# Kernel tuning notes

Hardware: AMD Instinct MI355X
Metric: run time of the kernel (lower is better)

## Reference

```python
import jax, jax.numpy as jnp
import numpy as np
import math

D_EMBED = 1536
N_HEADS = 12
D_AUG = D_EMBED // 3          # 512
HEAD_DIM = D_EMBED // N_HEADS # 128
ROPE_BASE = 10000.0


def apply_rope(x):
    # x: [B, S, H, D], interleaved-pair RoPE (torchtune convention)
    B, S, H, D = x.shape
    half = D // 2
    freqs = 1.0 / (ROPE_BASE ** (jnp.arange(0, D, 2, dtype=jnp.float32) / D))  # [half]
    ang = jnp.arange(S, dtype=jnp.float32)[:, None] * freqs[None, :]           # [S, half]
    cos = jnp.cos(ang)[None, :, None, :]  # [1,S,1,half]
    sin = jnp.sin(ang)[None, :, None, :]
    xr = x.reshape(B, S, H, half, 2)
    x1, x2 = xr[..., 0], xr[..., 1]
    out = jnp.stack([x1 * cos - x2 * sin, x1 * sin + x2 * cos], axis=-1)
    return out.reshape(B, S, H, D).astype(x.dtype)


def setup_inputs() -> dict:
    key = jax.random.key(0)
    ks = jax.random.split(key, 7)
    B, S = 2, 2048
    s = 0.02
    return {
        "q": jax.random.normal(ks[0], (B, S, D_EMBED), jnp.float32),
        "k": jax.random.normal(ks[1], (B, S, D_EMBED), jnp.float32),
        "v": jax.random.normal(ks[2], (B, S, D_EMBED), jnp.float32),
        "W_q": jax.random.normal(ks[3], (D_EMBED, D_EMBED), jnp.float32) * s,
        "W_k": jax.random.normal(ks[4], (D_EMBED, D_EMBED), jnp.float32) * s,
        "W_v": jax.random.normal(ks[5], (D_AUG, D_AUG), jnp.float32) * s,
        "W_o": jax.random.normal(ks[6], (D_EMBED, D_EMBED), jnp.float32) * s,
    }


def reference(q, k, v, W_q, W_k, W_v, W_o):
    # Dropout layers are identity in eval mode.
    B, S, _ = q.shape
    qh = q @ W_q.T                                     # [B,S,D]
    kh = k @ W_k.T
    v_mid = v[:, :, D_AUG:2 * D_AUG] @ W_v.T           # [B,S,D_AUG]
    vh = jnp.concatenate(
        [v_mid, jnp.zeros_like(v_mid), jnp.zeros_like(v_mid)], axis=-1)  # [B,S,D]

    qh = qh.reshape(B, S, N_HEADS, HEAD_DIM)
    kh = kh.reshape(B, S, N_HEADS, HEAD_DIM)
    vh = vh.reshape(B, S, N_HEADS, HEAD_DIM)

    qh = apply_rope(qh)
    kh = apply_rope(kh)

    scores = jnp.einsum('bqhd,bkhd->bhqk', qh, kh) / math.sqrt(HEAD_DIM)
    causal = jnp.triu(jnp.ones((S, S), dtype=bool), k=1)
    scores = jnp.where(causal[None, None], -jnp.inf, scores)
    probs = jax.nn.softmax(scores, axis=-1)

    attn = jnp.einsum('bhqk,bkhd->bqhd', probs, vh).reshape(B, S, D_EMBED)
    return attn @ W_o.T
```

## Files before the change

kernel.cpp:

```cpp
#include <hip/hip_runtime.h>
#include <hip/hip_bf16.h>

typedef __attribute__((ext_vector_type(8))) short short8;
typedef __attribute__((ext_vector_type(4))) short short4v;
typedef __attribute__((ext_vector_type(4))) float f32x4;

__device__ __forceinline__ short f2bf(float f) {
    union { float f; unsigned u; } v; v.f = f;
    unsigned r = (v.u + 0x7fffu + ((v.u >> 16) & 1u)) >> 16;
    return (short)r;
}
__device__ __forceinline__ float bf2f(short s) {
    union { unsigned u; float f; } v; v.u = ((unsigned)(unsigned short)s) << 16;
    return v.f;
}
__device__ __forceinline__ f32x4 zero4() { f32x4 z = {0.f, 0.f, 0.f, 0.f}; return z; }

__device__ __forceinline__ void gl16(const void* g, void* l) {
    __builtin_amdgcn_global_load_lds(
        (const __attribute__((address_space(1))) void*)g,
        (__attribute__((address_space(3))) void*)l, 16, 0, 0);
}

__global__ __launch_bounds__(256) void convertA_kernel(
    const float* __restrict__ q, const float* __restrict__ k,
    const float* __restrict__ Wq, const float* __restrict__ Wk,
    short* __restrict__ qb, short* __restrict__ kb,
    short* __restrict__ Wqb, short* __restrict__ Wkb)
{
    const int e0 = (blockIdx.x * 256 + threadIdx.x) * 8;
    const float* src; short* dst; int n;
    switch (blockIdx.z) {
    case 0:  n = 6291456; src = q + e0;  dst = qb;  break;
    case 1:  n = 6291456; src = k + e0;  dst = kb;  break;
    case 2:  n = 786432;  src = Wq + e0; dst = Wqb; break;
    default: n = 786432;  src = Wk + e0; dst = Wkb; break;
    }
    if (e0 >= n) return;
    float4 f0 = ((const float4*)src)[0];
    float4 f1 = ((const float4*)src)[1];
    short8 o;
    o[0]=f2bf(f0.x); o[1]=f2bf(f0.y); o[2]=f2bf(f0.z); o[3]=f2bf(f0.w);
    o[4]=f2bf(f1.x); o[5]=f2bf(f1.y); o[6]=f2bf(f1.z); o[7]=f2bf(f1.w);
    *(short8*)(dst + e0) = o;
}

template<bool ROPE>
__device__ __forceinline__ void gemm97_bf16out(
    const short* __restrict__ A, const short* __restrict__ B, short* __restrict__ Cp,
    int K, int lda, int ldb, int ldc, short* As, short* Bs)
{
    const int bm = blockIdx.y * 128;
    const int bn = blockIdx.x * 128;
    const int tid = threadIdx.x;
    const int w = tid >> 6;
    const int lane = tid & 63;
    const int l15 = lane & 15;
    const int quad = lane >> 4;
    const int wm = (w >> 1) * 64;
    const int wn = (w & 1) * 64;

    const int srow = w * 32 + (lane >> 2);
    const int scol = (lane & 3) * 8;
    const short* ga = A + (size_t)(bm + srow) * lda + scol;
    const short* gb = B + (size_t)(bn + srow) * ldb + scol;

    f32x4 acc[4][4];
#pragma unroll
    for (int i = 0; i < 4; i++)
#pragma unroll
        for (int j = 0; j < 4; j++) acc[i][j] = zero4();

    for (int k0 = 0; k0 < K; k0 += 64) {
        __syncthreads();
#pragma unroll
        for (int p = 0; p < 2; p++) {
            gl16(ga + k0 + p * 32,                    &As[p * 4096 + (w * 32) * 32]);
            gl16(ga + k0 + p * 32 + (size_t)16 * lda, &As[p * 4096 + (w * 32 + 16) * 32]);
            gl16(gb + k0 + p * 32,                    &Bs[p * 4096 + (w * 32) * 32]);
            gl16(gb + k0 + p * 32 + (size_t)16 * ldb, &Bs[p * 4096 + (w * 32 + 16) * 32]);
        }
        __syncthreads();

        short8 af[2][4], bf[2][4];
#pragma unroll
        for (int p = 0; p < 2; p++) {
#pragma unroll
            for (int i = 0; i < 4; i++)
                af[p][i] = *(const short8*)&As[p * 4096 + (wm + i * 16 + l15) * 32 + quad * 8];
#pragma unroll
            for (int j = 0; j < 4; j++)
                bf[p][j] = *(const short8*)&Bs[p * 4096 + (wn + j * 16 + l15) * 32 + quad * 8];
        }
#pragma unroll
        for (int i = 0; i < 4; i++)
#pragma unroll
            for (int j = 0; j < 4; j++) {
                acc[i][j] = __builtin_amdgcn_mfma_f32_16x16x32_bf16(af[0][i], bf[0][j], acc[i][j], 0, 0, 0);
                acc[i][j] = __builtin_amdgcn_mfma_f32_16x16x32_bf16(af[1][i], bf[1][j], acc[i][j], 0, 0, 0);
            }
    }

#pragma unroll
    for (int i = 0; i < 4; i++)
#pragma unroll
        for (int j = 0; j < 4; j++) {
            const int col = bn + wn + j * 16 + l15;
            const int row0 = bm + wm + i * 16 + quad * 4;
            if constexpr (ROPE) {
                const int pairi = (col & 127) >> 1;
                const float freq = exp2f(-(float)(2 * pairi) * (13.287712379549449f / 128.0f));
                const bool even = (l15 & 1) == 0;
#pragma unroll
                for (int r = 0; r < 4; r++) {
                    const float own = acc[i][j][r];
                    const float other = __shfl_xor(own, 1, 64);
                    const float pos = (float)((row0 + r) & 2047);
                    const float ang = pos * freq;
                    const float n = rintf(ang * 0.15915494309189535f);
                    const float rr = (ang - n * 6.28125f) - n * 1.9353071795864769e-3f;
                    float s, c;
                    __sincosf(rr, &s, &c);
                    const float x1 = even ? own : other;
                    const float x2 = even ? other : own;
                    const float res = even ? (x1 * c - x2 * s) : (x1 * s + x2 * c);
                    Cp[(size_t)(row0 + r) * ldc + col] = f2bf(res);
                }
            } else {
#pragma unroll
                for (int r = 0; r < 4; r++)
                    Cp[(size_t)(row0 + r) * ldc + col] = f2bf(acc[i][j][r]);
            }
        }
}

__device__ __forceinline__ void gemm_f32_bt_T(
    const float* __restrict__ A, const float* __restrict__ Bw, short* __restrict__ Cp,
    int K, int lda, int ldb, int ldc, short* As, short* Bs)
{
    const int bm = blockIdx.y * 128;
    const int bn = blockIdx.x * 128;
    const int tid = threadIdx.x;
    const int w = tid >> 6;
    const int lane = tid & 63;
    const int l15 = lane & 15;
    const int quad = lane >> 4;
    const int wm = (w >> 1) * 64;
    const int wn = (w & 1) * 64;
    const int srow = tid >> 1;
    const int scol = (tid & 1) * 16;

    f32x4 acc[4][4];
#pragma unroll
    for (int i = 0; i < 4; i++)
#pragma unroll
        for (int j = 0; j < 4; j++) acc[i][j] = zero4();

    for (int k0 = 0; k0 < K; k0 += 32) {
        __syncthreads();
        {
            const float* src = A + (size_t)(bm + srow) * lda + k0 + scol;
            short* dst = &As[srow * 40 + scol];
            const float4* s4 = (const float4*)src;
            float4 f0 = s4[0], f1 = s4[1], f2 = s4[2], f3 = s4[3];
            short8 t0, t1;
            t0[0]=f2bf(f0.x); t0[1]=f2bf(f0.y); t0[2]=f2bf(f0.z); t0[3]=f2bf(f0.w);
            t0[4]=f2bf(f1.x); t0[5]=f2bf(f1.y); t0[6]=f2bf(f1.z); t0[7]=f2bf(f1.w);
            t1[0]=f2bf(f2.x); t1[1]=f2bf(f2.y); t1[2]=f2bf(f2.z); t1[3]=f2bf(f2.w);
            t1[4]=f2bf(f3.x); t1[5]=f2bf(f3.y); t1[6]=f2bf(f3.z); t1[7]=f2bf(f3.w);
            *(short8*)dst = t0; *(short8*)(dst + 8) = t1;
        }
        {
            const float* src = Bw + (size_t)(bn + srow) * ldb + k0 + scol;
            short* dst = &Bs[srow * 40 + scol];
            const float4* s4 = (const float4*)src;
            float4 f0 = s4[0], f1 = s4[1], f2 = s4[2], f3 = s4[3];
            short8 t0, t1;
            t0[0]=f2bf(f0.x); t0[1]=f2bf(f0.y); t0[2]=f2bf(f0.z); t0[3]=f2bf(f0.w);
            t0[4]=f2bf(f1.x); t0[5]=f2bf(f1.y); t0[6]=f2bf(f1.z); t0[7]=f2bf(f1.w);
            t1[0]=f2bf(f2.x); t1[1]=f2bf(f2.y); t1[2]=f2bf(f2.z); t1[3]=f2bf(f2.w);
            t1[4]=f2bf(f3.x); t1[5]=f2bf(f3.y); t1[6]=f2bf(f3.z); t1[7]=f2bf(f3.w);
            *(short8*)dst = t0; *(short8*)(dst + 8) = t1;
        }
        __syncthreads();

        short8 af[4], bfr[4];
#pragma unroll
        for (int i = 0; i < 4; i++)
            af[i] = *(const short8*)&As[(wm + i * 16 + l15) * 40 + quad * 8];
#pragma unroll
        for (int j = 0; j < 4; j++)
            bfr[j] = *(const short8*)&Bs[(wn + j * 16 + l15) * 40 + quad * 8];
#pragma unroll
        for (int i = 0; i < 4; i++)
#pragma unroll
            for (int j = 0; j < 4; j++)
                acc[i][j] = __builtin_amdgcn_mfma_f32_16x16x32_bf16(af[i], bfr[j], acc[i][j], 0, 0, 0);
    }

#pragma unroll
    for (int i = 0; i < 4; i++)
#pragma unroll
        for (int j = 0; j < 4; j++) {
            const int col = bn + wn + j * 16 + l15;
            const int row0 = bm + wm + i * 16 + quad * 4;
            short4v p;
#pragma unroll
            for (int r = 0; r < 4; r++) p[r] = f2bf(acc[i][j][r]);
            *(short4v*)&Cp[(size_t)col * ldc + row0] = p;
        }
}

__device__ __forceinline__ void gemm_mixed_f32out(
    const short* __restrict__ A, const float* __restrict__ Bw, float* __restrict__ Cp,
    int K, int lda, int ldb, int ldc, short* As, short* Bs)
{
    const int bm = blockIdx.y * 128;
    const int bn = blockIdx.x * 128;
    const int tid = threadIdx.x;
    const int w = tid >> 6;
    const int lane = tid & 63;
    const int l15 = lane & 15;
    const int quad = lane >> 4;
    const int wm = (w >> 1) * 64;
    const int wn = (w & 1) * 64;
    const int srow = tid >> 1;
    const int scol = (tid & 1) * 16;

    f32x4 acc[4][4];
#pragma unroll
    for (int i = 0; i < 4; i++)
#pragma unroll
        for (int j = 0; j < 4; j++) acc[i][j] = zero4();

    for (int k0 = 0; k0 < K; k0 += 32) {
        __syncthreads();
        {
            const short* src = A + (size_t)(bm + srow) * lda + k0 + scol;
            short* dst = &As[srow * 40 + scol];
            const uint4* s4 = (const uint4*)src;
            uint4 a = s4[0], b = s4[1];
            *(uint4*)dst = a; *(uint4*)(dst + 8) = b;
        }
        {
            const float* src = Bw + (size_t)(bn + srow) * ldb + k0 + scol;
            short* dst = &Bs[srow * 40 + scol];
            const float4* s4 = (const float4*)src;
            float4 f0 = s4[0], f1 = s4[1], f2 = s4[2], f3 = s4[3];
            short8 t0, t1;
            t0[0]=f2bf(f0.x); t0[1]=f2bf(f0.y); t0[2]=f2bf(f0.z); t0[3]=f2bf(f0.w);
            t0[4]=f2bf(f1.x); t0[5]=f2bf(f1.y); t0[6]=f2bf(f1.z); t0[7]=f2bf(f1.w);
            t1[0]=f2bf(f2.x); t1[1]=f2bf(f2.y); t1[2]=f2bf(f2.z); t1[3]=f2bf(f2.w);
            t1[4]=f2bf(f3.x); t1[5]=f2bf(f3.y); t1[6]=f2bf(f3.z); t1[7]=f2bf(f3.w);
            *(short8*)dst = t0; *(short8*)(dst + 8) = t1;
        }
        __syncthreads();

        short8 af[4], bfr[4];
#pragma unroll
        for (int i = 0; i < 4; i++)
            af[i] = *(const short8*)&As[(wm + i * 16 + l15) * 40 + quad * 8];
#pragma unroll
        for (int j = 0; j < 4; j++)
            bfr[j] = *(const short8*)&Bs[(wn + j * 16 + l15) * 40 + quad * 8];
#pragma unroll
        for (int i = 0; i < 4; i++)
#pragma unroll
            for (int j = 0; j < 4; j++)
                acc[i][j] = __builtin_amdgcn_mfma_f32_16x16x32_bf16(af[i], bfr[j], acc[i][j], 0, 0, 0);
    }

#pragma unroll
    for (int i = 0; i < 4; i++)
#pragma unroll
        for (int j = 0; j < 4; j++) {
            const int col = bn + wn + j * 16 + l15;
            const int row0 = bm + wm + i * 16 + quad * 4;
#pragma unroll
            for (int r = 0; r < 4; r++)
                Cp[(size_t)(row0 + r) * ldc + col] = acc[i][j][r];
        }
}

__global__ __launch_bounds__(256) void proj_kernel(
    const short* __restrict__ qb, const short* __restrict__ kb, const float* __restrict__ v,
    const short* __restrict__ Wqb, const short* __restrict__ Wkb, const float* __restrict__ Wv,
    short* __restrict__ qh, short* __restrict__ kh, short* __restrict__ vT)
{
    __shared__ short smem[2][8192];
    switch (blockIdx.z) {
    case 0:  gemm97_bf16out<true>(qb, Wqb, qh, 1536, 1536, 1536, 512, smem[0], smem[1]); break;
    case 1:  gemm97_bf16out<true>(kb, Wkb, kh, 1536, 1536, 1536, 512, smem[0], smem[1]); break;
    default: gemm_f32_bt_T(v + 512, Wv, vT, 512, 1536, 512, 4096, smem[0], smem[1]); break;
    }
}

__global__ __launch_bounds__(256) void outproj_kernel(
    const short* __restrict__ attn, const float* __restrict__ Wo, float* __restrict__ out)
{
    __shared__ short smem[2][5120];
    gemm_mixed_f32out(attn, Wo, out, 512, 512, 1536, 1536, smem[0], smem[1]);
}

__global__ __launch_bounds__(256, 4) void flash_kernel(
    const short* __restrict__ qh, const short* __restrict__ kh,
    const short* __restrict__ vT, short* __restrict__ attn)
{
    __shared__ float Os[4][16][128];
    __shared__ short Ps[4][16 * 40];
    __shared__ float Lp[4][16];

    const int id = blockIdx.x;
    const int hb = id & 7;
    const int b = hb & 1;
    const int h = hb >> 1;
    const int s = id >> 3;
    const int m = s & 31;
    const int g = s >> 5;
    const int base = (g >> 1) * 32 + m;
    const int qt = (g & 1) ? (127 - base) : base;
    const int tid = threadIdx.x;
    const int w = tid >> 6;
    const int lane = tid & 63;
    const int l15 = lane & 15;
    const int quad = lane >> 4;

    const float scale = 0.08838834764831845f;
    const float MFIX = 24.0f;
    const short* kbp = kh + (size_t)(b * 2048) * 512 + h * 128;
    const short* vbp = vT + (size_t)(h * 128) * 4096 + b * 2048;
    short* pw = &Ps[w][0];

    const int q0 = qt * 16;
    const int ntiles = (q0 + 47) >> 5;

    const short* qrow = qh + (size_t)(b * 2048 + q0 + l15) * 512 + h * 128;
    short8 aq[4];
#pragma unroll
    for (int kk = 0; kk < 4; kk++)
        aq[kk] = *(const short8*)&qrow[kk * 32 + quad * 8];

    f32x4 o[8];
#pragma unroll
    for (int dt = 0; dt < 8; dt++) o[dt] = zero4();
    float lsum[4] = {0.f, 0.f, 0.f, 0.f};

    for (int t = w; t < ntiles; t += 4) {
        const int kb0 = t * 32;

        f32x4 sc[2];
#pragma unroll
        for (int ct = 0; ct < 2; ct++) {
            sc[ct] = zero4();
            const short* kr = kbp + (size_t)(kb0 + ct * 16 + l15) * 512;
#pragma unroll
            for (int kk = 0; kk < 4; kk++) {
                short8 bk = *(const short8*)&kr[kk * 32 + quad * 8];
                sc[ct] = __builtin_amdgcn_mfma_f32_16x16x32_bf16(aq[kk], bk, sc[ct], 0, 0, 0);
            }
        }

        short8 bv[8];
#pragma unroll
        for (int dt = 0; dt < 8; dt++)
            bv[dt] = *(const short8*)&vbp[(size_t)(dt * 16 + l15) * 4096 + kb0 + quad * 8];

        const int rbase = q0 + quad * 4;
        float p[2][4];
#pragma unroll
        for (int ct = 0; ct < 2; ct++) {
            const int kcol = kb0 + ct * 16 + l15;
#pragma unroll
            for (int r = 0; r < 4; r++) {
                const float e = __expf(sc[ct][r] * scale - MFIX);
                const float pv = (kcol > rbase + r) ? 0.0f : e;
                p[ct][r] = pv;
                lsum[r] += pv;
            }
        }

#pragma unroll
        for (int ct = 0; ct < 2; ct++)
#pragma unroll
            for (int r = 0; r < 4; r++)
                pw[(quad * 4 + r) * 40 + ct * 16 + l15] = f2bf(p[ct][r]);
        short8 ap = *(const short8*)&pw[l15 * 40 + quad * 8];

#pragma unroll
        for (int dt = 0; dt < 8; dt++)
            o[dt] = __builtin_amdgcn_mfma_f32_16x16x32_bf16(ap, bv[dt], o[dt], 0, 0, 0);
    }

#pragma unroll
    for (int r = 0; r < 4; r++) {
        float vsum = lsum[r];
#pragma unroll
        for (int off = 1; off < 16; off <<= 1)
            vsum += __shfl_xor(vsum, off, 64);
        if (l15 == 0) Lp[w][quad * 4 + r] = vsum;
#pragma unroll
        for (int dt = 0; dt < 8; dt++)
            Os[w][quad * 4 + r][dt * 16 + l15] = o[dt][r];
    }
    __syncthreads();

    {
        const int row = tid >> 4;
        const int d0 = (tid & 15) * 8;
        const float L = Lp[0][row] + Lp[1][row] + Lp[2][row] + Lp[3][row];
        const float rL = 1.0f / L;
        short8 ov;
#pragma unroll
        for (int j = 0; j < 8; j++) {
            const float osum = Os[0][row][d0 + j] + Os[1][row][d0 + j]
                             + Os[2][row][d0 + j] + Os[3][row][d0 + j];
            ov[j] = f2bf(osum * rL);
        }
        *(short8*)&attn[(size_t)(b * 2048 + q0 + row) * 512 + h * 128 + d0] = ov;
    }
}

extern "C" void kernel_launch(void* const* d_in, const int* in_sizes, int n_in,
                              void* d_out, int out_size, void* d_ws, size_t ws_size,
                              hipStream_t stream) {
    const float* q  = (const float*)d_in[0];
    const float* k  = (const float*)d_in[1];
    const float* v  = (const float*)d_in[2];
    const float* Wq = (const float*)d_in[3];
    const float* Wk = (const float*)d_in[4];
    const float* Wv = (const float*)d_in[5];
    const float* Wo = (const float*)d_in[6];
    float* out = (float*)d_out;

    const size_t MB = 1024 * 1024;
    char* ws = (char*)d_ws;
    short* qh   = (short*)(ws);
    short* kh   = (short*)(ws + 4 * MB);
    short* vT   = (short*)(ws + 8 * MB);
    short* Wqb  = (short*)(ws + 12 * MB);
    short* Wkb  = (short*)(ws + 13 * MB + 512 * 1024);
    short* attn = (short*)(ws + 12 * MB);
    short* qb   = (short*)d_out;
    short* kb   = (short*)((char*)d_out + 12 * MB);

    convertA_kernel<<<dim3(3072, 1, 4), 256, 0, stream>>>(q, k, Wq, Wk, qb, kb, Wqb, Wkb);
    proj_kernel<<<dim3(4, 32, 3), 256, 0, stream>>>(qb, kb, v, Wqb, Wkb, Wv, qh, kh, vT);
    flash_kernel<<<dim3(1024, 1, 1), 256, 0, stream>>>(qh, kh, vT, attn);
    outproj_kernel<<<dim3(12, 32, 1), 256, 0, stream>>>(attn, Wo, out);
}
```

Measured before the change: 256.7 us.

## Store K and V in MFMA-fragment layout and halve projection M-tile

The K and V projection epilogues now write outputs in a pre-swizzled fragment layout, 32-key tiles of 4096 shorts. The flash kernel can then load each MFMA operand as one contiguous 16-byte-per-lane read, instead of strided row gathers across 512- or 4096-element strides. The projection GEMMs also drop from 128-row to 64-row tiles, doubling the grid to improve occupancy and load balance. The trade-off is scattered short stores in the K epilogue and less reuse per block in the projection GEMMs.

```diff
diff --git a/kernel.cpp b/kernel.cpp
--- a/kernel.cpp
+++ b/kernel.cpp
@@ -45,29 +45,30 @@
     *(short8*)(dst + e0) = o;
 }
 
-template<bool ROPE>
-__device__ __forceinline__ void gemm97_bf16out(
+template<int MODE>
+__device__ __forceinline__ void gemm97_bm64(
     const short* __restrict__ A, const short* __restrict__ B, short* __restrict__ Cp,
     int K, int lda, int ldb, int ldc, short* As, short* Bs)
 {
-    const int bm = blockIdx.y * 128;
+    const int bm = blockIdx.y * 64;
     const int bn = blockIdx.x * 128;
     const int tid = threadIdx.x;
     const int w = tid >> 6;
     const int lane = tid & 63;
     const int l15 = lane & 15;
     const int quad = lane >> 4;
-    const int wm = (w >> 1) * 64;
+    const int wm = (w >> 1) * 32;
     const int wn = (w & 1) * 64;
 
-    const int srow = w * 32 + (lane >> 2);
-    const int scol = (lane & 3) * 8;
-    const short* ga = A + (size_t)(bm + srow) * lda + scol;
-    const short* gb = B + (size_t)(bn + srow) * ldb + scol;
-
-    f32x4 acc[4][4];
-#pragma unroll
-    for (int i = 0; i < 4; i++)
+    const int srA = w * 16 + (lane >> 2);
+    const int srB = w * 32 + (lane >> 2);
+    const int sc  = (lane & 3) * 8;
+    const short* ga = A + (size_t)(bm + srA) * lda + sc;
+    const short* gb = B + (size_t)(bn + srB) * ldb + sc;
+
+    f32x4 acc[2][4];
+#pragma unroll
+    for (int i = 0; i < 2; i++)
 #pragma unroll
         for (int j = 0; j < 4; j++) acc[i][j] = zero4();
 
@@ -75,25 +76,24 @@
         __syncthreads();
 #pragma unroll
         for (int p = 0; p < 2; p++) {
-            gl16(ga + k0 + p * 32,                    &As[p * 4096 + (w * 32) * 32]);
-            gl16(ga + k0 + p * 32 + (size_t)16 * lda, &As[p * 4096 + (w * 32 + 16) * 32]);
+            gl16(ga + k0 + p * 32,                    &As[p * 2048 + (w * 16) * 32]);
             gl16(gb + k0 + p * 32,                    &Bs[p * 4096 + (w * 32) * 32]);
             gl16(gb + k0 + p * 32 + (size_t)16 * ldb, &Bs[p * 4096 + (w * 32 + 16) * 32]);
         }
         __syncthreads();
 
-        short8 af[2][4], bf[2][4];
+        short8 af[2][2], bf[2][4];
 #pragma unroll
         for (int p = 0; p < 2; p++) {
 #pragma unroll
-            for (int i = 0; i < 4; i++)
-                af[p][i] = *(const short8*)&As[p * 4096 + (wm + i * 16 + l15) * 32 + quad * 8];
+            for (int i = 0; i < 2; i++)
+                af[p][i] = *(const short8*)&As[p * 2048 + (wm + i * 16 + l15) * 32 + quad * 8];
 #pragma unroll
             for (int j = 0; j < 4; j++)
                 bf[p][j] = *(const short8*)&Bs[p * 4096 + (wn + j * 16 + l15) * 32 + quad * 8];
         }
 #pragma unroll
-        for (int i = 0; i < 4; i++)
+        for (int i = 0; i < 2; i++)
 #pragma unroll
             for (int j = 0; j < 4; j++) {
                 acc[i][j] = __builtin_amdgcn_mfma_f32_16x16x32_bf16(af[0][i], bf[0][j], acc[i][j], 0, 0, 0);
@@ -102,42 +102,140 @@
     }
 
 #pragma unroll
-    for (int i = 0; i < 4; i++)
+    for (int i = 0; i < 2; i++)
 #pragma unroll
         for (int j = 0; j < 4; j++) {
             const int col = bn + wn + j * 16 + l15;
             const int row0 = bm + wm + i * 16 + quad * 4;
-            if constexpr (ROPE) {
-                const int pairi = (col & 127) >> 1;
-                const float freq = exp2f(-(float)(2 * pairi) * (13.287712379549449f / 128.0f));
-                const bool even = (l15 & 1) == 0;
-#pragma unroll
-                for (int r = 0; r < 4; r++) {
-                    const float own = acc[i][j][r];
-                    const float other = __shfl_xor(own, 1, 64);
-                    const float pos = (float)((row0 + r) & 2047);
-                    const float ang = pos * freq;
-                    const float n = rintf(ang * 0.15915494309189535f);
-                    const float rr = (ang - n * 6.28125f) - n * 1.9353071795864769e-3f;
-                    float s, c;
-                    __sincosf(rr, &s, &c);
-                    const float x1 = even ? own : other;
-                    const float x2 = even ? other : own;
-                    const float res = even ? (x1 * c - x2 * s) : (x1 * s + x2 * c);
+            const int pairi = (col & 127) >> 1;
+            const float freq = exp2f(-(float)(2 * pairi) * (13.287712379549449f / 128.0f));
+            const bool even = (l15 & 1) == 0;
+#pragma unroll
+            for (int r = 0; r < 4; r++) {
+                const float own = acc[i][j][r];
+                const float other = __shfl_xor(own, 1, 64);
+                const float pos = (float)((row0 + r) & 2047);
+                const float ang = pos * freq;
+                const float n = rintf(ang * 0.15915494309189535f);
+                const float rr = (ang - n * 6.28125f) - n * 1.9353071795864769e-3f;
+                float s, c;
+                __sincosf(rr, &s, &c);
+                const float x1 = even ? own : other;
+                const float x2 = even ? other : own;
+                const float res = even ? (x1 * c - x2 * s) : (x1 * s + x2 * c);
+                if constexpr (MODE == 1) {
                     Cp[(size_t)(row0 + r) * ldc + col] = f2bf(res);
+                } else {
+                    const int seq = row0 + r;
+                    const int b_ = seq >> 11;
+                    const int s2 = seq & 2047;
+                    Cp[(size_t)(b_ * 4 + (col >> 7)) * 262144 + (s2 >> 5) * 4096
+                       + ((s2 >> 4) & 1) * 2048 + ((col >> 5) & 3) * 512
+                       + ((col >> 3) & 3) * 128 + (s2 & 15) * 8 + (col & 7)] = f2bf(res);
                 }
-            } else {
-#pragma unroll
-                for (int r = 0; r < 4; r++)
-                    Cp[(size_t)(row0 + r) * ldc + col] = f2bf(acc[i][j][r]);
             }
         }
 }
 
-__device__ __forceinline__ void gemm_f32_bt_T(
+__device__ __forceinline__ void gemm_f32T_vF(
     const float* __restrict__ A, const float* __restrict__ Bw, short* __restrict__ Cp,
-    int K, int lda, int ldb, int ldc, short* As, short* Bs)
-{
+    int K, int lda, int ldb, short* As, short* Bs)
+{
+    const int bm = blockIdx.y * 64;
+    const int bn = blockIdx.x * 128;
+    const int tid = threadIdx.x;
+    const int w = tid >> 6;
+    const int lane = tid & 63;
+    const int l15 = lane & 15;
+    const int quad = lane >> 4;
+    const int wm = (w >> 1) * 32;
+    const int wn = (w & 1) * 64;
+    const int srA = tid >> 2;
+    const int scA = (tid & 3) * 8;
+    const int srB = tid >> 1;
+    const int scB = (tid & 1) * 16;
+
+    f32x4 acc[2][4];
+#pragma unroll
+    for (int i = 0; i < 2; i++)
+#pragma unroll
+        for (int j = 0; j < 4; j++) acc[i][j] = zero4();
+
+    for (int k0 = 0; k0 < K; k0 += 32) {
+        __syncthreads();
+        {
+            const float* src = A + (size_t)(bm + srA) * lda + k0 + scA;
+            short* dst = &As[srA * 40 + scA];
+            const float4* s4 = (const float4*)src;
+            float4 f0 = s4[0], f1 = s4[1];
+            short8 t0;
+            t0[0]=f2bf(f0.x); t0[1]=f2bf(f0.y); t0[2]=f2bf(f0.z); t0[3]=f2bf(f0.w);
+            t0[4]=f2bf(f1.x); t0[5]=f2bf(f1.y); t0[6]=f2bf(f1.z); t0[7]=f2bf(f1.w);
+            *(short8*)dst = t0;
+        }
+        {
+            const float* src = Bw + (size_t)(bn + srB) * ldb + k0 + scB;
+            short* dst = &Bs[srB * 40 + scB];
+            const float4* s4 = (const float4*)src;
+            float4 f0 = s4[0], f1 = s4[1], f2 = s4[2], f3 = s4[3];
+            short8 t0, t1;
+            t0[0]=f2bf(f0.x); t0[1]=f2bf(f0.y); t0[2]=f2bf(f0.z); t0[3]=f2bf(f0.w);
+            t0[4]=f2bf(f1.x); t0[5]=f2bf(f1.y); t0[6]=f2bf(f1.z); t0[7]=f2bf(f1.w);
+            t1[0]=f2bf(f2.x); t1[1]=f2bf(f2.y); t1[2]=f2bf(f2.z); t1[3]=f2bf(f2.w);
+            t1[4]=f2bf(f3.x); t1[5]=f2bf(f3.y); t1[6]=f2bf(f3.z); t1[7]=f2bf(f3.w);
+            *(short8*)dst = t0; *(short8*)(dst + 8) = t1;
+        }
+        __syncthreads();
+
+        short8 af[2], bfr[4];
+#pragma unroll
+        for (int i = 0; i < 2; i++)
+            af[i] = *(const short8*)&As[(wm + i * 16 + l15) * 40 + quad * 8];
+#pragma unroll
+        for (int j = 0; j < 4; j++)
+            bfr[j] = *(const short8*)&Bs[(wn + j * 16 + l15) * 40 + quad * 8];
+#pragma unroll
+        for (int i = 0; i < 2; i++)
+#pragma unroll
+            for (int j = 0; j < 4; j++)
+                acc[i][j] = __builtin_amdgcn_mfma_f32_16x16x32_bf16(af[i], bfr[j], acc[i][j], 0, 0, 0);
+    }
+
+#pragma unroll
+    for (int i = 0; i < 2; i++)
+#pragma unroll
+        for (int j = 0; j < 4; j++) {
+            const int col = bn + wn + j * 16 + l15;
+            const int row0 = bm + wm + i * 16 + quad * 4;
+            const int b_ = row0 >> 11;
+            const int s2 = row0 & 2047;
+            short4v p;
+#pragma unroll
+            for (int r = 0; r < 4; r++) p[r] = f2bf(acc[i][j][r]);
+            const size_t addr = (size_t)(b_ * 4 + (col >> 7)) * 262144 + (s2 >> 5) * 4096
+                              + ((col >> 4) & 7) * 512 + ((s2 >> 3) & 3) * 128
+                              + (col & 15) * 8 + (s2 & 7);
+            *(short4v*)&Cp[addr] = p;
+        }
+}
+
+__global__ __launch_bounds__(256) void proj_kernel(
+    const short* __restrict__ qb, const short* __restrict__ kb, const float* __restrict__ v,
+    const short* __restrict__ Wqb, const short* __restrict__ Wkb, const float* __restrict__ Wv,
+    short* __restrict__ qh, short* __restrict__ khF, short* __restrict__ vF)
+{
+    __shared__ short smem[12288];
+    switch (blockIdx.z) {
+    case 0:  gemm97_bm64<1>(qb, Wqb, qh,  1536, 1536, 1536, 512, smem, smem + 4096); break;
+    case 1:  gemm97_bm64<2>(kb, Wkb, khF, 1536, 1536, 1536, 512, smem, smem + 4096); break;
+    default: gemm_f32T_vF(v + 512, Wv, vF, 512, 1536, 512, smem, smem + 2560); break;
+    }
+}
+
+__global__ __launch_bounds__(256) void outproj_kernel(
+    const short* __restrict__ attn, const float* __restrict__ Wo, float* __restrict__ out)
+{
+    __shared__ short smem[2][5120];
     const int bm = blockIdx.y * 128;
     const int bn = blockIdx.x * 128;
     const int tid = threadIdx.x;
@@ -149,6 +247,9 @@
     const int wn = (w & 1) * 64;
     const int srow = tid >> 1;
     const int scol = (tid & 1) * 16;
+    short* As = smem[0];
+    short* Bs = smem[1];
+    const int K = 512, lda = 512, ldb = 1536, ldc = 1536;
 
     f32x4 acc[4][4];
 #pragma unroll
@@ -159,19 +260,14 @@
     for (int k0 = 0; k0 < K; k0 += 32) {
         __syncthreads();
         {
-            const float* src = A + (size_t)(bm + srow) * lda + k0 + scol;
+            const short* src = attn + (size_t)(bm + srow) * lda + k0 + scol;
             short* dst = &As[srow * 40 + scol];
-            const float4* s4 = (const float4*)src;
-            float4 f0 = s4[0], f1 = s4[1], f2 = s4[2], f3 = s4[3];
-            short8 t0, t1;
-            t0[0]=f2bf(f0.x); t0[1]=f2bf(f0.y); t0[2]=f2bf(f0.z); t0[3]=f2bf(f0.w);
-            t0[4]=f2bf(f1.x); t0[5]=f2bf(f1.y); t0[6]=f2bf(f1.z); t0[7]=f2bf(f1.w);
-            t1[0]=f2bf(f2.x); t1[1]=f2bf(f2.y); t1[2]=f2bf(f2.z); t1[3]=f2bf(f2.w);
-            t1[4]=f2bf(f3.x); t1[5]=f2bf(f3.y); t1[6]=f2bf(f3.z); t1[7]=f2bf(f3.w);
-            *(short8*)dst = t0; *(short8*)(dst + 8) = t1;
+            const uint4* s4 = (const uint4*)src;
+            uint4 a = s4[0], b = s4[1];
+            *(uint4*)dst = a; *(uint4*)(dst + 8) = b;
         }
         {
-            const float* src = Bw + (size_t)(bn + srow) * ldb + k0 + scol;
+            const float* src = Wo + (size_t)(bn + srow) * ldb + k0 + scol;
             short* dst = &Bs[srow * 40 + scol];
             const float4* s4 = (const float4*)src;
             float4 f0 = s4[0], f1 = s4[1], f2 = s4[2], f3 = s4[3];
@@ -204,107 +300,15 @@
         for (int j = 0; j < 4; j++) {
             const int col = bn + wn + j * 16 + l15;
             const int row0 = bm + wm + i * 16 + quad * 4;
-            short4v p;
-#pragma unroll
-            for (int r = 0; r < 4; r++) p[r] = f2bf(acc[i][j][r]);
-            *(short4v*)&Cp[(size_t)col * ldc + row0] = p;
-        }
-}
-
-__device__ __forceinline__ void gemm_mixed_f32out(
-    const short* __restrict__ A, const float* __restrict__ Bw, float* __restrict__ Cp,
-    int K, int lda, int ldb, int ldc, short* As, short* Bs)
-{
-    const int bm = blockIdx.y * 128;
-    const int bn = blockIdx.x * 128;
-    const int tid = threadIdx.x;
-    const int w = tid >> 6;
-    const int lane = tid & 63;
-    const int l15 = lane & 15;
-    const int quad = lane >> 4;
-    const int wm = (w >> 1) * 64;
-    const int wn = (w & 1) * 64;
-    const int srow = tid >> 1;
-    const int scol = (tid & 1) * 16;
-
-    f32x4 acc[4][4];
-#pragma unroll
-    for (int i = 0; i < 4; i++)
-#pragma unroll
-        for (int j = 0; j < 4; j++) acc[i][j] = zero4();
-
-    for (int k0 = 0; k0 < K; k0 += 32) {
-        __syncthreads();
-        {
-            const short* src = A + (size_t)(bm + srow) * lda + k0 + scol;
-            short* dst = &As[srow * 40 + scol];
-            const uint4* s4 = (const uint4*)src;
-            uint4 a = s4[0], b = s4[1];
-            *(uint4*)dst = a; *(uint4*)(dst + 8) = b;
-        }
-        {
-            const float* src = Bw + (size_t)(bn + srow) * ldb + k0 + scol;
-            short* dst = &Bs[srow * 40 + scol];
-            const float4* s4 = (const float4*)src;
-            float4 f0 = s4[0], f1 = s4[1], f2 = s4[2], f3 = s4[3];
-            short8 t0, t1;
-            t0[0]=f2bf(f0.x); t0[1]=f2bf(f0.y); t0[2]=f2bf(f0.z); t0[3]=f2bf(f0.w);
-            t0[4]=f2bf(f1.x); t0[5]=f2bf(f1.y); t0[6]=f2bf(f1.z); t0[7]=f2bf(f1.w);
-            t1[0]=f2bf(f2.x); t1[1]=f2bf(f2.y); t1[2]=f2bf(f2.z); t1[3]=f2bf(f2.w);
-            t1[4]=f2bf(f3.x); t1[5]=f2bf(f3.y); t1[6]=f2bf(f3.z); t1[7]=f2bf(f3.w);
-            *(short8*)dst = t0; *(short8*)(dst + 8) = t1;
-        }
-        __syncthreads();
-
-        short8 af[4], bfr[4];
-#pragma unroll
-        for (int i = 0; i < 4; i++)
-            af[i] = *(const short8*)&As[(wm + i * 16 + l15) * 40 + quad * 8];
-#pragma unroll
-        for (int j = 0; j < 4; j++)
-            bfr[j] = *(const short8*)&Bs[(wn + j * 16 + l15) * 40 + quad * 8];
-#pragma unroll
-        for (int i = 0; i < 4; i++)
-#pragma unroll
-            for (int j = 0; j < 4; j++)
-                acc[i][j] = __builtin_amdgcn_mfma_f32_16x16x32_bf16(af[i], bfr[j], acc[i][j], 0, 0, 0);
-    }
-
-#pragma unroll
-    for (int i = 0; i < 4; i++)
-#pragma unroll
-        for (int j = 0; j < 4; j++) {
-            const int col = bn + wn + j * 16 + l15;
-            const int row0 = bm + wm + i * 16 + quad * 4;
 #pragma unroll
             for (int r = 0; r < 4; r++)
-                Cp[(size_t)(row0 + r) * ldc + col] = acc[i][j][r];
-        }
-}
-
-__global__ __launch_bounds__(256) void proj_kernel(
-    const short* __restrict__ qb, const short* __restrict__ kb, const float* __restrict__ v,
-    const short* __restrict__ Wqb, const short* __restrict__ Wkb, const float* __restrict__ Wv,
-    short* __restrict__ qh, short* __restrict__ kh, short* __restrict__ vT)
-{
-    __shared__ short smem[2][8192];
-    switch (blockIdx.z) {
-    case 0:  gemm97_bf16out<true>(qb, Wqb, qh, 1536, 1536, 1536, 512, smem[0], smem[1]); break;
-    case 1:  gemm97_bf16out<true>(kb, Wkb, kh, 1536, 1536, 1536, 512, smem[0], smem[1]); break;
-    default: gemm_f32_bt_T(v + 512, Wv, vT, 512, 1536, 512, 4096, smem[0], smem[1]); break;
-    }
-}
-
-__global__ __launch_bounds__(256) void outproj_kernel(
-    const short* __restrict__ attn, const float* __restrict__ Wo, float* __restrict__ out)
-{
-    __shared__ short smem[2][5120];
-    gemm_mixed_f32out(attn, Wo, out, 512, 512, 1536, 1536, smem[0], smem[1]);
+                out[(size_t)(row0 + r) * ldc + col] = acc[i][j][r];
+        }
 }
 
 __global__ __launch_bounds__(256, 4) void flash_kernel(
-    const short* __restrict__ qh, const short* __restrict__ kh,
-    const short* __restrict__ vT, short* __restrict__ attn)
+    const short* __restrict__ qh, const short* __restrict__ khF,
+    const short* __restrict__ vF, short* __restrict__ attn)
 {
     __shared__ float Os[4][16][128];
     __shared__ short Ps[4][16 * 40];
@@ -327,9 +331,6 @@
 
     const float scale = 0.08838834764831845f;
     const float MFIX = 24.0f;
-    const short* kbp = kh + (size_t)(b * 2048) * 512 + h * 128;
-    const short* vbp = vT + (size_t)(h * 128) * 4096 + b * 2048;
-    short* pw = &Ps[w][0];
 
     const int q0 = qt * 16;
     const int ntiles = (q0 + 47) >> 5;
@@ -340,22 +341,28 @@
     for (int kk = 0; kk < 4; kk++)
         aq[kk] = *(const short8*)&qrow[kk * 32 + quad * 8];
 
+    const short* kfb = khF + (size_t)(b * 4 + h) * 262144 + lane * 8;
+    const short* vfb = vF  + (size_t)(b * 4 + h) * 262144 + lane * 8;
+
     f32x4 o[8];
 #pragma unroll
     for (int dt = 0; dt < 8; dt++) o[dt] = zero4();
     float lsum[4] = {0.f, 0.f, 0.f, 0.f};
 
+    short* pw = &Ps[w][0];
+
     for (int t = w; t < ntiles; t += 4) {
         const int kb0 = t * 32;
+        const short* kt_ = kfb + t * 4096;
+        const short* vt_ = vfb + t * 4096;
 
         f32x4 sc[2];
 #pragma unroll
         for (int ct = 0; ct < 2; ct++) {
             sc[ct] = zero4();
-            const short* kr = kbp + (size_t)(kb0 + ct * 16 + l15) * 512;
 #pragma unroll
             for (int kk = 0; kk < 4; kk++) {
-                short8 bk = *(const short8*)&kr[kk * 32 + quad * 8];
+                short8 bk = *(const short8*)&kt_[ct * 2048 + kk * 512];
                 sc[ct] = __builtin_amdgcn_mfma_f32_16x16x32_bf16(aq[kk], bk, sc[ct], 0, 0, 0);
             }
         }
@@ -363,7 +370,7 @@
         short8 bv[8];
 #pragma unroll
         for (int dt = 0; dt < 8; dt++)
-            bv[dt] = *(const short8*)&vbp[(size_t)(dt * 16 + l15) * 4096 + kb0 + quad * 8];
+            bv[dt] = *(const short8*)&vt_[dt * 512];
 
         const int rbase = q0 + quad * 4;
         float p[2][4];
@@ -435,8 +442,8 @@
     const size_t MB = 1024 * 1024;
     char* ws = (char*)d_ws;
     short* qh   = (short*)(ws);
-    short* kh   = (short*)(ws + 4 * MB);
-    short* vT   = (short*)(ws + 8 * MB);
+    short* khF  = (short*)(ws + 4 * MB);
+    short* vF   = (short*)(ws + 8 * MB);
     short* Wqb  = (short*)(ws + 12 * MB);
     short* Wkb  = (short*)(ws + 13 * MB + 512 * 1024);
     short* attn = (short*)(ws + 12 * MB);
@@ -444,7 +451,7 @@
     short* kb   = (short*)((char*)d_out + 12 * MB);
 
     convertA_kernel<<<dim3(3072, 1, 4), 256, 0, stream>>>(q, k, Wq, Wk, qb, kb, Wqb, Wkb);
-    proj_kernel<<<dim3(4, 32, 3), 256, 0, stream>>>(qb, kb, v, Wqb, Wkb, Wv, qh, kh, vT);
-    flash_kernel<<<dim3(1024, 1, 1), 256, 0, stream>>>(qh, kh, vT, attn);
+    proj_kernel<<<dim3(4, 64, 3), 256, 0, stream>>>(qb, kb, v, Wqb, Wkb, Wv, qh, khF, vF);
+    flash_kernel<<<dim3(1024, 1, 1), 256, 0, stream>>>(qh, khF, vF, attn);
     outproj_kernel<<<dim3(12, 32, 1), 256, 0, stream>>>(attn, Wo, out);
 }
```

After: 222.8 us. -13.2%, faster.
